# Optimization experiments

Measured on AMD Instinct MI355X. Metric: run time of the kernel, lower is better.

The kernel has to match this reference:

```python
import jax, jax.numpy as jnp
import numpy as np

B, S, D, H = 2, 2048, 1024, 16
DH = D // H  # head_dim = 64


def setup_inputs() -> dict:
    key = jax.random.key(0)
    ks = jax.random.split(key, 12)
    sd = 0.02
    return {
        "query": jax.random.normal(ks[0], (B, S, D), jnp.float32),
        "value": jax.random.normal(ks[1], (B, S, D), jnp.float32),
        "Wq": jax.random.normal(ks[2], (D, D), jnp.float32) * sd,
        "bq": jnp.zeros((D,), jnp.float32),
        "Wk": jax.random.normal(ks[3], (D, DH), jnp.float32) * sd,
        "bk": jnp.zeros((DH,), jnp.float32),
        "Wv": jax.random.normal(ks[4], (D, DH), jnp.float32) * sd,
        "bv": jnp.zeros((DH,), jnp.float32),
        "Wo": jax.random.normal(ks[5], (D, D), jnp.float32) * sd,
        "bo": jnp.zeros((D,), jnp.float32),
    }


def reference(query, value, Wq, bq, Wk, bk, Wv, bv, Wo, bo):
    b, s, d = query.shape
    # per-head queries: (B, H, S, DH)
    Q = (query @ Wq + bq).reshape(b, s, H, DH).transpose(0, 2, 1, 3)
    # single shared K/V head: (B, S, DH)
    K = value @ Wk + bk
    V = value @ Wv + bv
    scale = 1.0 / jnp.sqrt(jnp.asarray(DH, Q.dtype))
    # broadcast shared K over all query heads: (B, H, S, S)
    scores = jnp.einsum("bhsd,btd->bhst", Q, K) * scale
    weights = jax.nn.softmax(scores, axis=-1)
    # (B, H, S, DH)
    attn = jnp.einsum("bhst,btd->bhsd", weights, V)
    concat = attn.transpose(0, 2, 1, 3).reshape(b, s, d)
    return concat @ Wo + bo
```

## Files before the change

kernel.cpp:

```cpp
#include <hip/hip_runtime.h>
#include <hip/hip_bf16.h>
#include <cstdint>

#define S_LEN 2048
#define D_MODEL 1024
#define NHEAD 16
#define DHEAD 64
#define BATCH 2

typedef __attribute__((ext_vector_type(4))) __bf16 bf16x4v;
typedef __attribute__((ext_vector_type(8))) __bf16 bf16x8v;
typedef __attribute__((ext_vector_type(16))) float f32x16;
typedef const __attribute__((address_space(1))) uint32_t gu32;
typedef __attribute__((address_space(3))) uint32_t lu32;

#define QSCALE 0.18033688011112042f

__device__ __forceinline__ int perm4(int gidx) {
    return (gidx & ~3) | ((gidx & 1) << 1) | ((gidx >> 1) & 1);
}
__device__ __forceinline__ int permk(int k) {
    return (k & ~12) | ((k & 4) << 1) | ((k & 8) >> 1);
}

__global__ __launch_bounds__(256) void prep_all(
    const float* __restrict__ query,
    const float* __restrict__ Wq, const float* __restrict__ Wo,
    const float* __restrict__ Wk, const float* __restrict__ Wv,
    __hip_bfloat16* __restrict__ Qin,
    __hip_bfloat16* __restrict__ Wqt, __hip_bfloat16* __restrict__ Wohit,
    __hip_bfloat16* __restrict__ Wkvt)
{
    const int bid = blockIdx.x;
    const int tid = threadIdx.x;
    if (bid < 4096) {
        const int idx = bid * 256 + tid;
        const float4 v = reinterpret_cast<const float4*>(query)[idx];
        bf16x4v o = { (__bf16)v.x, (__bf16)v.y, (__bf16)v.z, (__bf16)v.w };
        *reinterpret_cast<bf16x4v*>(Qin + (size_t)perm4(idx) * 4) = o;
        return;
    }
    const int b2 = bid - 4096;
    const int bx = b2 & 31, by = (b2 >> 5) & 31, z = b2 >> 10;
    const float* W;
    __hip_bfloat16* T;
    int wcols, trowoff;
    if (z == 0)      { W = Wq; T = Wqt;   wcols = 1024; trowoff = 0; }
    else if (z == 1) { W = Wo; T = Wohit; wcols = 1024; trowoff = 0; }
    else if (z == 2) { W = Wk; T = Wkvt;  wcols = 64;   trowoff = 0; }
    else             { W = Wv; T = Wkvt;  wcols = 64;   trowoff = 64; }
    if (bx * 32 >= wcols) return;

    __shared__ float ld[32][33];
    const int jj = tid & 31;
#pragma unroll
    for (int ii = 0; ii < 4; ++ii) {
        const int rr = (tid >> 5) * 4 + ii;
        ld[rr][jj] = W[(size_t)(by * 32 + rr) * wcols + bx * 32 + jj];
    }
    __syncthreads();
#pragma unroll
    for (int ii = 0; ii < 4; ++ii) {
        const int rr = (tid >> 5) * 4 + ii;
        T[(size_t)(trowoff + bx * 32 + rr) * 1024 + by * 32 + permk(jj)] =
            __float2bfloat16(ld[jj][rr]);
    }
}

__global__ __launch_bounds__(512, 1) void qproj_projkv(
    const __hip_bfloat16* __restrict__ Qin,
    const __hip_bfloat16* __restrict__ Wqt,
    const float* __restrict__ bq,
    __hip_bfloat16* __restrict__ Qbf,
    const float* __restrict__ value,
    const __hip_bfloat16* __restrict__ Wkvt,
    const float* __restrict__ bk, const float* __restrict__ bv,
    __hip_bfloat16* __restrict__ Kb,
    __hip_bfloat16* __restrict__ Vt)
{
    __shared__ __align__(16) char lds[131072];
    const int bid = blockIdx.x;
    const int tid = threadIdx.x;

    if (bid < 64) {
        const int unit = tid >> 8;
        const int ltid = tid & 255;
        const int w = ltid >> 6, lane = ltid & 63;
        const int g = lane >> 5, r = lane & 31;
        const int rowBase = bid * 64 + unit * 32;
        char* ub = lds + unit * 65536;

        auto stage = [&](int buf, int t) {
            const int kk = t * 64;
            char* dst = ub + buf * 24576;
#pragma unroll
            for (int j = 0; j < 2; ++j) {
                const int oo  = j * 4096 + ltid * 16;
                const int row = oo >> 8;
                const int cb  = (oo & 255) ^ ((row & 7) << 4);
                __builtin_amdgcn_global_load_lds(
                    (gu32*)((const char*)value + (size_t)(rowBase + row) * 4096 + kk * 4 + cb),
                    (lu32*)(dst + oo), 16, 0, 0);
            }
#pragma unroll
            for (int j = 0; j < 4; ++j) {
                const int oo  = j * 4096 + ltid * 16;
                const int row = oo >> 7;
                const int cb  = (oo & 127) ^ ((row & 7) << 4);
                __builtin_amdgcn_global_load_lds(
                    (gu32*)((const char*)Wkvt + (size_t)row * 2048 + kk * 2 + cb),
                    (lu32*)(dst + 8192 + oo), 16, 0, 0);
            }
        };

        f32x16 acc;
#pragma unroll
        for (int i = 0; i < 16; ++i) acc[i] = 0.f;

        stage(0, 0);

        for (int t = 0; t < 16; ++t) {
            const int cur = t & 1;
            if (t < 15) {
                stage(cur ^ 1, t + 1);
                asm volatile("s_waitcnt vmcnt(6)" ::: "memory");
            } else {
                asm volatile("s_waitcnt vmcnt(0)" ::: "memory");
            }
            asm volatile("s_barrier" ::: "memory");

            const char* ab = ub + cur * 24576;
            const char* bb = ab + 8192;

#pragma unroll
            for (int ks = 0; ks < 4; ++ks) {
                const int sza = (r & 7) << 4;
                const char* pa = ab + r * 256;
                const float4 x0 = *reinterpret_cast<const float4*>(
                    pa + ((ks * 64 + g * 16) ^ sza));
                const float4 x1 = *reinterpret_cast<const float4*>(
                    pa + ((ks * 64 + 32 + g * 16) ^ sza));
                bf16x8v af = {(__bf16)x0.x, (__bf16)x0.y, (__bf16)x0.z, (__bf16)x0.w,
                              (__bf16)x1.x, (__bf16)x1.y, (__bf16)x1.z, (__bf16)x1.w};
                bf16x8v bf = *reinterpret_cast<const bf16x8v*>(
                    bb + (w * 32 + r) * 128 + ((ks * 32 + g * 16) ^ sza));
                acc = __builtin_amdgcn_mfma_f32_32x32x16_bf16(af, bf, acc, 0, 0, 0);
            }
            asm volatile("s_barrier" ::: "memory");
        }

        __syncthreads();
        float* ep = reinterpret_cast<float*>(ub);
#pragma unroll
        for (int reg = 0; reg < 16; ++reg) {
            const int m = (reg & 3) + 8 * (reg >> 2) + 4 * g;
            ep[m * 132 + w * 32 + r] = acc[reg];
        }
        __syncthreads();

        {
            const int m  = ltid >> 3;
            const int g0 = (ltid & 7) * 2;
#pragma unroll
            for (int j = 0; j < 2; ++j) {
                const int gsrc = g0 + j;
                bf16x4v o4;
#pragma unroll
                for (int i2 = 0; i2 < 4; ++i2)
                    o4[i2] = (__bf16)(ep[m * 132 + gsrc * 4 + i2] + bk[gsrc * 4 + i2]);
                *reinterpret_cast<bf16x4v*>(
                    Kb + (size_t)(rowBase + m) * 64 + perm4(gsrc) * 4) = o4;
            }
        }
        {
            const int vc = ltid >> 2;
            const int g0 = (ltid & 3) * 2;
            const int batch = rowBase >> 11;
            const float bvv = bv[vc];
#pragma unroll
            for (int j = 0; j < 2; ++j) {
                const int gsrc = g0 + j;
                bf16x4v o4;
#pragma unroll
                for (int i2 = 0; i2 < 4; ++i2)
                    o4[i2] = (__bf16)(ep[(gsrc * 4 + i2) * 132 + 64 + vc] + bvv);
                *reinterpret_cast<bf16x4v*>(
                    Vt + ((size_t)(batch * 64 + vc)) * 2048 + (rowBase & 2047) + perm4(gsrc) * 4) = o4;
            }
        }
        return;
    }

    const int lin = bid - 64;
    const int w = tid >> 6, lane = tid & 63;
    const int g = lane >> 5, r = lane & 31;
    const int wr = w >> 2, wc = w & 3;
    const int swz = (lin & 7) * 32 + (lin >> 3);
    const int rowBase = (swz >> 3) * 128;
    const int colBase = (swz & 7) * 128;

    auto stage = [&](int buf, int t) {
        const int kk = t * 64;
        char* dst = lds + buf * 32768;
#pragma unroll
        for (int j = 0; j < 2; ++j) {
            const int oo  = j * 8192 + tid * 16;
            const int row = oo >> 7;
            const int cb  = (oo & 127) ^ ((row & 7) << 4);
            __builtin_amdgcn_global_load_lds(
                (gu32*)((const char*)Qin + (size_t)(rowBase + row) * 2048 + kk * 2 + cb),
                (lu32*)(dst + oo), 16, 0, 0);
            __builtin_amdgcn_global_load_lds(
                (gu32*)((const char*)Wqt + (size_t)(colBase + row) * 2048 + kk * 2 + cb),
                (lu32*)(dst + 16384 + oo), 16, 0, 0);
        }
    };

    f32x16 acc[2];
#pragma unroll
    for (int i = 0; i < 16; ++i) { acc[0][i] = 0.f; acc[1][i] = 0.f; }

    stage(0, 0); stage(1, 1); stage(2, 2);

    for (int t = 0; t < 16; ++t) {
        if (t <= 13)      { asm volatile("s_waitcnt vmcnt(8)" ::: "memory"); }
        else if (t == 14) { asm volatile("s_waitcnt vmcnt(4)" ::: "memory"); }
        else              { asm volatile("s_waitcnt vmcnt(0)" ::: "memory"); }
        asm volatile("s_barrier" ::: "memory");

        if (t + 3 < 16) stage((t + 3) & 3, t + 3);

        const char* ahb = lds + (t & 3) * 32768;
        const char* bb  = ahb + 16384;

        __builtin_amdgcn_s_setprio(1);
#pragma unroll
        for (int ks = 0; ks < 4; ++ks) {
            bf16x8v a[2], bfr;
#pragma unroll
            for (int mt = 0; mt < 2; ++mt) {
                const int rowl = wr * 64 + mt * 32 + r;
                const int sz = (rowl & 7) << 4;
                a[mt] = *reinterpret_cast<const bf16x8v*>(
                    ahb + rowl * 128 + ((ks * 32 + g * 16) ^ sz));
            }
            {
                const int rowl = wc * 32 + r;
                const int sz = (rowl & 7) << 4;
                bfr = *reinterpret_cast<const bf16x8v*>(
                    bb + rowl * 128 + ((ks * 32 + g * 16) ^ sz));
            }
#pragma unroll
            for (int mt = 0; mt < 2; ++mt)
                acc[mt] = __builtin_amdgcn_mfma_f32_32x32x16_bf16(a[mt], bfr, acc[mt], 0, 0, 0);
        }
        __builtin_amdgcn_s_setprio(0);
    }

    const int col = colBase + wc * 32 + r;
    const int colp = permk(col);
    const float bvv = bq[col];
#pragma unroll
    for (int mt = 0; mt < 2; ++mt)
#pragma unroll
        for (int reg = 0; reg < 16; ++reg) {
            const int row = rowBase + wr * 64 + mt * 32 + (reg & 3) + 8 * (reg >> 2) + 4 * g;
            Qbf[(size_t)row * 1024 + colp] =
                (__hip_bfloat16)((acc[mt][reg] + bvv) * QSCALE);
        }
}

__global__ __launch_bounds__(512, 1) void gemm_oproj(
    const __hip_bfloat16* __restrict__ Ahi, const __hip_bfloat16* __restrict__ Alo,
    const __hip_bfloat16* __restrict__ Bhi,
    const float* __restrict__ bias, float* __restrict__ C)
{
    constexpr int BUFSZ = 49152;
    __shared__ __align__(16) char lds[147456];

    const int tid = threadIdx.x;
    const int w = tid >> 6, lane = tid & 63;
    const int g = lane >> 5, r = lane & 31;
    const int wr = w >> 2, wc = w & 3;
    const int lin = blockIdx.y * 8 + blockIdx.x;
    const int swz = (lin & 7) * 32 + (lin >> 3);
    const int rowBase = (swz >> 3) * 128;
    const int colBase = (swz & 7) * 128;

    auto stage = [&](int buf, int t) {
        const int kk = t * 64;
        char* dst = lds + buf * BUFSZ;
#pragma unroll
        for (int j = 0; j < 2; ++j) {
            const int oo  = j * 8192 + tid * 16;
            const int row = oo >> 7;
            const int cb  = (oo & 127) ^ ((row & 7) << 4);
            __builtin_amdgcn_global_load_lds(
                (gu32*)((const char*)Ahi + (size_t)(rowBase + row) * 2048 + kk * 2 + cb),
                (lu32*)(dst + oo), 16, 0, 0);
            __builtin_amdgcn_global_load_lds(
                (gu32*)((const char*)Alo + (size_t)(rowBase + row) * 2048 + kk * 2 + cb),
                (lu32*)(dst + 16384 + oo), 16, 0, 0);
            __builtin_amdgcn_global_load_lds(
                (gu32*)((const char*)Bhi + (size_t)(colBase + row) * 2048 + kk * 2 + cb),
                (lu32*)(dst + 32768 + oo), 16, 0, 0);
        }
    };

    f32x16 acc[2];
#pragma unroll
    for (int i = 0; i < 16; ++i) { acc[0][i] = 0.f; acc[1][i] = 0.f; }

    stage(0, 0); stage(1, 1);
    int b_cur = 0, b_nxt = 1, b_stg = 2;

    for (int t = 0; t < 16; ++t) {
        if (t < 15) { asm volatile("s_waitcnt vmcnt(6)" ::: "memory"); }
        else        { asm volatile("s_waitcnt vmcnt(0)" ::: "memory"); }
        asm volatile("s_barrier" ::: "memory");

        if (t + 2 < 16) stage(b_stg, t + 2);

        const char* ahb = lds + b_cur * BUFSZ;
        const char* alb = ahb + 16384;
        const char* bb  = ahb + 32768;

        __builtin_amdgcn_s_setprio(1);
#pragma unroll
        for (int ks = 0; ks < 4; ++ks) {
            bf16x8v a[2], a2[2], bfr;
#pragma unroll
            for (int mt = 0; mt < 2; ++mt) {
                const int rowl = wr * 64 + mt * 32 + r;
                const int sz = (rowl & 7) << 4;
                a[mt]  = *reinterpret_cast<const bf16x8v*>(
                    ahb + rowl * 128 + ((ks * 32 + g * 16) ^ sz));
                a2[mt] = *reinterpret_cast<const bf16x8v*>(
                    alb + rowl * 128 + ((ks * 32 + g * 16) ^ sz));
            }
            {
                const int rowl = wc * 32 + r;
                const int sz = (rowl & 7) << 4;
                bfr = *reinterpret_cast<const bf16x8v*>(
                    bb + rowl * 128 + ((ks * 32 + g * 16) ^ sz));
            }
#pragma unroll
            for (int mt = 0; mt < 2; ++mt) {
                acc[mt] = __builtin_amdgcn_mfma_f32_32x32x16_bf16(a[mt],  bfr, acc[mt], 0, 0, 0);
                acc[mt] = __builtin_amdgcn_mfma_f32_32x32x16_bf16(a2[mt], bfr, acc[mt], 0, 0, 0);
            }
        }
        __builtin_amdgcn_s_setprio(0);

        const int tmp = b_cur; b_cur = b_nxt; b_nxt = b_stg; b_stg = tmp;
    }

    const int col = colBase + wc * 32 + r;
    const float bvv = bias[col];
#pragma unroll
    for (int mt = 0; mt < 2; ++mt)
#pragma unroll
        for (int reg = 0; reg < 16; ++reg) {
            const int row = rowBase + wr * 64 + mt * 32 + (reg & 3) + 8 * (reg >> 2) + 4 * g;
            C[(size_t)row * 1024 + col] = acc[mt][reg] + bvv;
        }
}

__global__ __launch_bounds__(256, 2) void mqa_attn_mfma(
    const __hip_bfloat16* __restrict__ Qbf,
    const __hip_bfloat16* __restrict__ Kbf,
    const __hip_bfloat16* __restrict__ Vt,
    __hip_bfloat16* __restrict__ Ahi,
    __hip_bfloat16* __restrict__ Alo)
{
    __shared__ __align__(16) char lds[65536];

    const int bh = blockIdx.y, b = bh >> 4, h = bh & 15;
    const int qt = blockIdx.x;
    const int tid = threadIdx.x;
    const int w = tid >> 6, lane = tid & 63;
    const int g = lane >> 5, q = lane & 31;

    bf16x8v qf[4];
    {
        const __hip_bfloat16* qp =
            Qbf + ((size_t)(b * S_LEN + qt * 128 + w * 32 + q)) * D_MODEL + h * DHEAD;
#pragma unroll
        for (int ks = 0; ks < 4; ++ks)
            qf[ks] = *reinterpret_cast<const bf16x8v*>(qp + ks * 16 + g * 8);
    }

    const bf16x8v onesf = {(__bf16)1.f, (__bf16)1.f, (__bf16)1.f, (__bf16)1.f,
                           (__bf16)1.f, (__bf16)1.f, (__bf16)1.f, (__bf16)1.f};
    f32x16 fzero;
#pragma unroll
    for (int i = 0; i < 16; ++i) fzero[i] = 0.f;

    int koff[2][4], voff[2][4];
#pragma unroll
    for (int mt = 0; mt < 2; ++mt) {
        const int key = mt * 32 + q;
        const int swzk = (key & 7) << 4;
#pragma unroll
        for (int ks = 0; ks < 4; ++ks) {
            koff[mt][ks] = key * 128 + ((ks * 32 + g * 16) ^ swzk);
            voff[mt][ks] = 8192 + key * 128 + ((ks * 32 + g * 16) ^ swzk);
        }
    }

    const char* kbase = (const char*)Kbf + (size_t)b * S_LEN * DHEAD * 2;
    const char* vbase = (const char*)Vt + (size_t)b * DHEAD * S_LEN * 2;

    auto stage = [&](int buf, int t0) {
        char* dst = lds + buf * 16384;
#pragma unroll
        for (int j = 0; j < 2; ++j) {
            const int oo = j * 4096 + tid * 16;
            const int rr = oo >> 7;
            const int cc = (oo & 127) ^ ((rr & 7) << 4);
            __builtin_amdgcn_global_load_lds(
                (gu32*)(kbase + (size_t)(t0 + rr) * 128 + cc),
                (lu32*)(dst + oo), 16, 0, 0);
            __builtin_amdgcn_global_load_lds(
                (gu32*)(vbase + (size_t)rr * (S_LEN * 2) + t0 * 2 + cc),
                (lu32*)(dst + 8192 + oo), 16, 0, 0);
        }
    };

    f32x16 oacc[2], oacc_l;
#pragma unroll
    for (int i = 0; i < 16; ++i) { oacc[0][i] = 0.f; oacc[1][i] = 0.f; oacc_l[i] = 0.f; }

    auto qkt = [&](f32x16 (&SD)[2], int buf) {
        const char* kb_ = lds + buf * 16384;
#pragma unroll
        for (int mt = 0; mt < 2; ++mt) {
            bf16x8v af0 = *reinterpret_cast<const bf16x8v*>(kb_ + koff[mt][0]);
            SD[mt] = __builtin_amdgcn_mfma_f32_32x32x16_bf16(af0, qf[0], fzero, 0, 0, 0);
#pragma unroll
            for (int ks = 1; ks < 4; ++ks) {
                bf16x8v af = *reinterpret_cast<const bf16x8v*>(kb_ + koff[mt][ks]);
                SD[mt] = __builtin_amdgcn_mfma_f32_32x32x16_bf16(af, qf[ks], SD[mt], 0, 0, 0);
            }
        }
    };

    auto smpv = [&](f32x16 (&SD)[2], int buf) {
#pragma unroll
        for (int mt = 0; mt < 2; ++mt)
#pragma unroll
            for (int r2 = 0; r2 < 16; ++r2)
                SD[mt][r2] = exp2f(SD[mt][r2]);

        bf16x8v pf[4];
#pragma unroll
        for (int ks = 0; ks < 4; ++ks)
#pragma unroll
            for (int e2 = 0; e2 < 8; ++e2)
                pf[ks][e2] = (__bf16)SD[ks >> 1][(ks & 1) * 8 + e2];

        const char* kb_ = lds + buf * 16384;
#pragma unroll
        for (int mt = 0; mt < 2; ++mt) {
#pragma unroll
            for (int ks = 0; ks < 4; ++ks) {
                bf16x8v af = *reinterpret_cast<const bf16x8v*>(kb_ + voff[mt][ks]);
                oacc[mt] = __builtin_amdgcn_mfma_f32_32x32x16_bf16(af, pf[ks], oacc[mt], 0, 0, 0);
            }
        }
#pragma unroll
        for (int ks = 0; ks < 4; ++ks)
            oacc_l = __builtin_amdgcn_mfma_f32_32x32x16_bf16(onesf, pf[ks], oacc_l, 0, 0, 0);
    };

    f32x16 sA[2], sB[2];

    stage(0, 0); stage(1, 64); stage(2, 128);
    asm volatile("s_waitcnt vmcnt(8)" ::: "memory");
    asm volatile("s_barrier" ::: "memory");
    qkt(sA, 0);

#define BODY(SB_, TILE_, BQ_, BP_, CUR, NXT, VMCSTR, DOSTAGE)               \
    {                                                                        \
        asm volatile("s_waitcnt vmcnt(" VMCSTR ")" ::: "memory");            \
        asm volatile("s_barrier" ::: "memory");                              \
        if (DOSTAGE) stage(SB_, TILE_);                                      \
        qkt(NXT, BQ_);                                                       \
        smpv(CUR, BP_);                                                      \
    }

    for (int ib = 0; ib < 7; ++ib) {
        const int t4 = ib * 4;
        BODY(3, (t4 + 3) * 64, 1, 0, sA, sB, "4", true);
        BODY(0, (t4 + 4) * 64, 2, 1, sB, sA, "4", true);
        BODY(1, (t4 + 5) * 64, 3, 2, sA, sB, "4", true);
        BODY(2, (t4 + 6) * 64, 0, 3, sB, sA, "4", true);
    }
    BODY(3, 31 * 64, 1, 0, sA, sB, "4", true);
    BODY(0, 0,       2, 1, sB, sA, "4", false);
    BODY(0, 0,       3, 2, sA, sB, "0", false);
#undef BODY
    smpv(sB, 3);

    const float inv = 1.f / oacc_l[0];
    __syncthreads();
    {
        float* ep = reinterpret_cast<float*>(lds) + w * 2080;
#pragma unroll
        for (int mt = 0; mt < 2; ++mt)
#pragma unroll
            for (int r = 0; r < 16; ++r) {
                const int d = mt * 32 + (r & 3) + ((r >> 2) * 8) + g * 4;
                ep[q * 65 + d] = oacc[mt][r] * inv;
            }
    }
    __syncthreads();

    const size_t obase = (size_t)(b * S_LEN + qt * 128) * D_MODEL + h * DHEAD;
    for (int i = tid; i < 128 * 16; i += 256) {
        const int rloc = i >> 4, G = i & 15;
        const float* src = reinterpret_cast<float*>(lds) + (rloc >> 5) * 2080 + (rloc & 31) * 65 + G * 4;
        const size_t o = obase + (size_t)rloc * D_MODEL + perm4(G) * 4;
        bf16x4v hv, lv;
#pragma unroll
        for (int j = 0; j < 4; ++j) {
            const float v = src[j];
            const float h2 = __bfloat162float(__float2bfloat16(v));
            hv[j] = (__bf16)h2;
            lv[j] = (__bf16)(v - h2);
        }
        *reinterpret_cast<bf16x4v*>(Ahi + o) = hv;
        *reinterpret_cast<bf16x4v*>(Alo + o) = lv;
    }
}

extern "C" void kernel_launch(void* const* d_in, const int* in_sizes, int n_in,
                              void* d_out, int out_size, void* d_ws, size_t ws_size,
                              hipStream_t stream)
{
    const float* query = (const float*)d_in[0];
    const float* value = (const float*)d_in[1];
    const float* Wq    = (const float*)d_in[2];
    const float* bq    = (const float*)d_in[3];
    const float* Wk    = (const float*)d_in[4];
    const float* bk    = (const float*)d_in[5];
    const float* Wv    = (const float*)d_in[6];
    const float* bv    = (const float*)d_in[7];
    const float* Wo    = (const float*)d_in[8];
    const float* bo    = (const float*)d_in[9];
    float* out = (float*)d_out;

    char* ws = (char*)d_ws;
    const size_t MB = 1024 * 1024;
    __hip_bfloat16* Qin   = (__hip_bfloat16*)(ws);
    __hip_bfloat16* AhiB  = (__hip_bfloat16*)(ws);
    __hip_bfloat16* Wqt   = (__hip_bfloat16*)(ws + 8 * MB);
    __hip_bfloat16* Qbf   = (__hip_bfloat16*)(ws + 10 * MB);
    __hip_bfloat16* AloB  = (__hip_bfloat16*)(ws + 10 * MB);
    __hip_bfloat16* Kbf   = (__hip_bfloat16*)(ws + 18 * MB);
    __hip_bfloat16* Vt    = (__hip_bfloat16*)(ws + 18 * MB + 524288);
    __hip_bfloat16* Wohit = (__hip_bfloat16*)(ws + 19 * MB);
    __hip_bfloat16* Wkvt  = (__hip_bfloat16*)(ws + 21 * MB);

    prep_all<<<dim3(8192), dim3(256), 0, stream>>>(
        query, Wq, Wo, Wk, Wv, Qin, Wqt, Wohit, Wkvt);

    qproj_projkv<<<dim3(320), dim3(512), 0, stream>>>(
        Qin, Wqt, bq, Qbf, value, Wkvt, bk, bv, Kbf, Vt);

    mqa_attn_mfma<<<dim3(S_LEN / 128, BATCH * NHEAD), dim3(256), 0, stream>>>(
        Qbf, Kbf, Vt, AhiB, AloB);

    gemm_oproj<<<dim3(8, 32), dim3(512), 0, stream>>>(
        AhiB, AloB, Wohit, bo, out);
}
```

Baseline: 109.3 us.

## Fuse query bf16 conversion into Q-proj GEMM and drop hi/lo split of attention output

The query fp32-to-bf16 conversion pass is removed; the Q-projection GEMM now stages fp32 query tiles into LDS and converts to bf16 while building MFMA fragments, with a 3-buffer pipeline. The attention output is now written as a single bf16 tensor instead of hi/lo split pairs, halving the MFMA work and A-loads in the output projection. This removes an extra global round-trip and redundant compute, at the cost of lower output-projection precision and more LDS traffic in the Q-projection.

```diff
diff --git a/kernel.cpp b/kernel.cpp
--- a/kernel.cpp
+++ b/kernel.cpp
@@ -23,25 +23,13 @@
     return (k & ~12) | ((k & 4) << 1) | ((k & 8) >> 1);
 }
 
-__global__ __launch_bounds__(256) void prep_all(
-    const float* __restrict__ query,
+__global__ __launch_bounds__(256) void prep_w(
     const float* __restrict__ Wq, const float* __restrict__ Wo,
     const float* __restrict__ Wk, const float* __restrict__ Wv,
-    __hip_bfloat16* __restrict__ Qin,
     __hip_bfloat16* __restrict__ Wqt, __hip_bfloat16* __restrict__ Wohit,
     __hip_bfloat16* __restrict__ Wkvt)
 {
-    const int bid = blockIdx.x;
-    const int tid = threadIdx.x;
-    if (bid < 4096) {
-        const int idx = bid * 256 + tid;
-        const float4 v = reinterpret_cast<const float4*>(query)[idx];
-        bf16x4v o = { (__bf16)v.x, (__bf16)v.y, (__bf16)v.z, (__bf16)v.w };
-        *reinterpret_cast<bf16x4v*>(Qin + (size_t)perm4(idx) * 4) = o;
-        return;
-    }
-    const int b2 = bid - 4096;
-    const int bx = b2 & 31, by = (b2 >> 5) & 31, z = b2 >> 10;
+    const int z = blockIdx.z;
     const float* W;
     __hip_bfloat16* T;
     int wcols, trowoff;
@@ -49,9 +37,11 @@
     else if (z == 1) { W = Wo; T = Wohit; wcols = 1024; trowoff = 0; }
     else if (z == 2) { W = Wk; T = Wkvt;  wcols = 64;   trowoff = 0; }
     else             { W = Wv; T = Wkvt;  wcols = 64;   trowoff = 64; }
+    const int bx = blockIdx.x, by = blockIdx.y;
     if (bx * 32 >= wcols) return;
 
     __shared__ float ld[32][33];
+    const int tid = threadIdx.x;
     const int jj = tid & 31;
 #pragma unroll
     for (int ii = 0; ii < 4; ++ii) {
@@ -68,7 +58,7 @@
 }
 
 __global__ __launch_bounds__(512, 1) void qproj_projkv(
-    const __hip_bfloat16* __restrict__ Qin,
+    const float* __restrict__ query,
     const __hip_bfloat16* __restrict__ Wqt,
     const float* __restrict__ bq,
     __hip_bfloat16* __restrict__ Qbf,
@@ -78,7 +68,7 @@
     __hip_bfloat16* __restrict__ Kb,
     __hip_bfloat16* __restrict__ Vt)
 {
-    __shared__ __align__(16) char lds[131072];
+    __shared__ __align__(16) char lds[147456];
     const int bid = blockIdx.x;
     const int tid = threadIdx.x;
 
@@ -201,18 +191,24 @@
 
     auto stage = [&](int buf, int t) {
         const int kk = t * 64;
-        char* dst = lds + buf * 32768;
+        char* dst = lds + buf * 49152;
+#pragma unroll
+        for (int j = 0; j < 4; ++j) {
+            const int oo  = j * 8192 + tid * 16;
+            const int row = oo >> 8;
+            const int cb  = (oo & 255) ^ ((row & 7) << 4);
+            __builtin_amdgcn_global_load_lds(
+                (gu32*)((const char*)query + (size_t)(rowBase + row) * 4096 + kk * 4 + cb),
+                (lu32*)(dst + oo), 16, 0, 0);
+        }
 #pragma unroll
         for (int j = 0; j < 2; ++j) {
             const int oo  = j * 8192 + tid * 16;
             const int row = oo >> 7;
             const int cb  = (oo & 127) ^ ((row & 7) << 4);
             __builtin_amdgcn_global_load_lds(
-                (gu32*)((const char*)Qin + (size_t)(rowBase + row) * 2048 + kk * 2 + cb),
-                (lu32*)(dst + oo), 16, 0, 0);
-            __builtin_amdgcn_global_load_lds(
                 (gu32*)((const char*)Wqt + (size_t)(colBase + row) * 2048 + kk * 2 + cb),
-                (lu32*)(dst + 16384 + oo), 16, 0, 0);
+                (lu32*)(dst + 32768 + oo), 16, 0, 0);
         }
     };
 
@@ -220,18 +216,18 @@
 #pragma unroll
     for (int i = 0; i < 16; ++i) { acc[0][i] = 0.f; acc[1][i] = 0.f; }
 
-    stage(0, 0); stage(1, 1); stage(2, 2);
+    stage(0, 0); stage(1, 1);
+    int b_cur = 0, b_nxt = 1, b_stg = 2;
 
     for (int t = 0; t < 16; ++t) {
-        if (t <= 13)      { asm volatile("s_waitcnt vmcnt(8)" ::: "memory"); }
-        else if (t == 14) { asm volatile("s_waitcnt vmcnt(4)" ::: "memory"); }
-        else              { asm volatile("s_waitcnt vmcnt(0)" ::: "memory"); }
+        if (t < 15) { asm volatile("s_waitcnt vmcnt(6)" ::: "memory"); }
+        else        { asm volatile("s_waitcnt vmcnt(0)" ::: "memory"); }
         asm volatile("s_barrier" ::: "memory");
 
-        if (t + 3 < 16) stage((t + 3) & 3, t + 3);
-
-        const char* ahb = lds + (t & 3) * 32768;
-        const char* bb  = ahb + 16384;
+        if (t + 2 < 16) stage(b_stg, t + 2);
+
+        const char* ab = lds + b_cur * 49152;
+        const char* bb = ab + 32768;
 
         __builtin_amdgcn_s_setprio(1);
 #pragma unroll
@@ -241,8 +237,13 @@
             for (int mt = 0; mt < 2; ++mt) {
                 const int rowl = wr * 64 + mt * 32 + r;
                 const int sz = (rowl & 7) << 4;
-                a[mt] = *reinterpret_cast<const bf16x8v*>(
-                    ahb + rowl * 128 + ((ks * 32 + g * 16) ^ sz));
+                const char* pa = ab + rowl * 256;
+                const float4 x0 = *reinterpret_cast<const float4*>(
+                    pa + ((ks * 64 + g * 16) ^ sz));
+                const float4 x1 = *reinterpret_cast<const float4*>(
+                    pa + ((ks * 64 + 32 + g * 16) ^ sz));
+                a[mt] = bf16x8v{(__bf16)x0.x, (__bf16)x0.y, (__bf16)x0.z, (__bf16)x0.w,
+                                (__bf16)x1.x, (__bf16)x1.y, (__bf16)x1.z, (__bf16)x1.w};
             }
             {
                 const int rowl = wc * 32 + r;
@@ -255,6 +256,8 @@
                 acc[mt] = __builtin_amdgcn_mfma_f32_32x32x16_bf16(a[mt], bfr, acc[mt], 0, 0, 0);
         }
         __builtin_amdgcn_s_setprio(0);
+
+        const int tmp = b_cur; b_cur = b_nxt; b_nxt = b_stg; b_stg = tmp;
     }
 
     const int col = colBase + wc * 32 + r;
@@ -271,12 +274,11 @@
 }
 
 __global__ __launch_bounds__(512, 1) void gemm_oproj(
-    const __hip_bfloat16* __restrict__ Ahi, const __hip_bfloat16* __restrict__ Alo,
+    const __hip_bfloat16* __restrict__ A,
     const __hip_bfloat16* __restrict__ Bhi,
     const float* __restrict__ bias, float* __restrict__ C)
 {
-    constexpr int BUFSZ = 49152;
-    __shared__ __align__(16) char lds[147456];
+    __shared__ __align__(16) char lds[131072];
 
     const int tid = threadIdx.x;
     const int w = tid >> 6, lane = tid & 63;
@@ -289,21 +291,18 @@
 
     auto stage = [&](int buf, int t) {
         const int kk = t * 64;
-        char* dst = lds + buf * BUFSZ;
+        char* dst = lds + buf * 32768;
 #pragma unroll
         for (int j = 0; j < 2; ++j) {
             const int oo  = j * 8192 + tid * 16;
             const int row = oo >> 7;
             const int cb  = (oo & 127) ^ ((row & 7) << 4);
             __builtin_amdgcn_global_load_lds(
-                (gu32*)((const char*)Ahi + (size_t)(rowBase + row) * 2048 + kk * 2 + cb),
+                (gu32*)((const char*)A + (size_t)(rowBase + row) * 2048 + kk * 2 + cb),
                 (lu32*)(dst + oo), 16, 0, 0);
             __builtin_amdgcn_global_load_lds(
-                (gu32*)((const char*)Alo + (size_t)(rowBase + row) * 2048 + kk * 2 + cb),
+                (gu32*)((const char*)Bhi + (size_t)(colBase + row) * 2048 + kk * 2 + cb),
                 (lu32*)(dst + 16384 + oo), 16, 0, 0);
-            __builtin_amdgcn_global_load_lds(
-                (gu32*)((const char*)Bhi + (size_t)(colBase + row) * 2048 + kk * 2 + cb),
-                (lu32*)(dst + 32768 + oo), 16, 0, 0);
         }
     };
 
@@ -311,32 +310,29 @@
 #pragma unroll
     for (int i = 0; i < 16; ++i) { acc[0][i] = 0.f; acc[1][i] = 0.f; }
 
-    stage(0, 0); stage(1, 1);
-    int b_cur = 0, b_nxt = 1, b_stg = 2;
+    stage(0, 0); stage(1, 1); stage(2, 2);
 
     for (int t = 0; t < 16; ++t) {
-        if (t < 15) { asm volatile("s_waitcnt vmcnt(6)" ::: "memory"); }
-        else        { asm volatile("s_waitcnt vmcnt(0)" ::: "memory"); }
+        if (t <= 13)      { asm volatile("s_waitcnt vmcnt(8)" ::: "memory"); }
+        else if (t == 14) { asm volatile("s_waitcnt vmcnt(4)" ::: "memory"); }
+        else              { asm volatile("s_waitcnt vmcnt(0)" ::: "memory"); }
         asm volatile("s_barrier" ::: "memory");
 
-        if (t + 2 < 16) stage(b_stg, t + 2);
-
-        const char* ahb = lds + b_cur * BUFSZ;
-        const char* alb = ahb + 16384;
-        const char* bb  = ahb + 32768;
+        if (t + 3 < 16) stage((t + 3) & 3, t + 3);
+
+        const char* ahb = lds + (t & 3) * 32768;
+        const char* bb  = ahb + 16384;
 
         __builtin_amdgcn_s_setprio(1);
 #pragma unroll
         for (int ks = 0; ks < 4; ++ks) {
-            bf16x8v a[2], a2[2], bfr;
+            bf16x8v a[2], bfr;
 #pragma unroll
             for (int mt = 0; mt < 2; ++mt) {
                 const int rowl = wr * 64 + mt * 32 + r;
                 const int sz = (rowl & 7) << 4;
-                a[mt]  = *reinterpret_cast<const bf16x8v*>(
+                a[mt] = *reinterpret_cast<const bf16x8v*>(
                     ahb + rowl * 128 + ((ks * 32 + g * 16) ^ sz));
-                a2[mt] = *reinterpret_cast<const bf16x8v*>(
-                    alb + rowl * 128 + ((ks * 32 + g * 16) ^ sz));
             }
             {
                 const int rowl = wc * 32 + r;
@@ -345,14 +341,10 @@
                     bb + rowl * 128 + ((ks * 32 + g * 16) ^ sz));
             }
 #pragma unroll
-            for (int mt = 0; mt < 2; ++mt) {
-                acc[mt] = __builtin_amdgcn_mfma_f32_32x32x16_bf16(a[mt],  bfr, acc[mt], 0, 0, 0);
-                acc[mt] = __builtin_amdgcn_mfma_f32_32x32x16_bf16(a2[mt], bfr, acc[mt], 0, 0, 0);
-            }
+            for (int mt = 0; mt < 2; ++mt)
+                acc[mt] = __builtin_amdgcn_mfma_f32_32x32x16_bf16(a[mt], bfr, acc[mt], 0, 0, 0);
         }
         __builtin_amdgcn_s_setprio(0);
-
-        const int tmp = b_cur; b_cur = b_nxt; b_nxt = b_stg; b_stg = tmp;
     }
 
     const int col = colBase + wc * 32 + r;
@@ -370,8 +362,7 @@
     const __hip_bfloat16* __restrict__ Qbf,
     const __hip_bfloat16* __restrict__ Kbf,
     const __hip_bfloat16* __restrict__ Vt,
-    __hip_bfloat16* __restrict__ Ahi,
-    __hip_bfloat16* __restrict__ Alo)
+    __hip_bfloat16* __restrict__ Ahi)
 {
     __shared__ __align__(16) char lds[65536];
 
@@ -521,16 +512,10 @@
         const int rloc = i >> 4, G = i & 15;
         const float* src = reinterpret_cast<float*>(lds) + (rloc >> 5) * 2080 + (rloc & 31) * 65 + G * 4;
         const size_t o = obase + (size_t)rloc * D_MODEL + perm4(G) * 4;
-        bf16x4v hv, lv;
-#pragma unroll
-        for (int j = 0; j < 4; ++j) {
-            const float v = src[j];
-            const float h2 = __bfloat162float(__float2bfloat16(v));
-            hv[j] = (__bf16)h2;
-            lv[j] = (__bf16)(v - h2);
-        }
+        bf16x4v hv;
+#pragma unroll
+        for (int j = 0; j < 4; ++j) hv[j] = (__bf16)src[j];
         *reinterpret_cast<bf16x4v*>(Ahi + o) = hv;
-        *reinterpret_cast<bf16x4v*>(Alo + o) = lv;
     }
 }
 
@@ -552,25 +537,23 @@
 
     char* ws = (char*)d_ws;
     const size_t MB = 1024 * 1024;
-    __hip_bfloat16* Qin   = (__hip_bfloat16*)(ws);
-    __hip_bfloat16* AhiB  = (__hip_bfloat16*)(ws);
+    __hip_bfloat16* Qbf   = (__hip_bfloat16*)(ws);
+    __hip_bfloat16* Abuf  = (__hip_bfloat16*)(ws);
     __hip_bfloat16* Wqt   = (__hip_bfloat16*)(ws + 8 * MB);
-    __hip_bfloat16* Qbf   = (__hip_bfloat16*)(ws + 10 * MB);
-    __hip_bfloat16* AloB  = (__hip_bfloat16*)(ws + 10 * MB);
-    __hip_bfloat16* Kbf   = (__hip_bfloat16*)(ws + 18 * MB);
-    __hip_bfloat16* Vt    = (__hip_bfloat16*)(ws + 18 * MB + 524288);
-    __hip_bfloat16* Wohit = (__hip_bfloat16*)(ws + 19 * MB);
-    __hip_bfloat16* Wkvt  = (__hip_bfloat16*)(ws + 21 * MB);
-
-    prep_all<<<dim3(8192), dim3(256), 0, stream>>>(
-        query, Wq, Wo, Wk, Wv, Qin, Wqt, Wohit, Wkvt);
+    __hip_bfloat16* Kbf   = (__hip_bfloat16*)(ws + 10 * MB);
+    __hip_bfloat16* Vt    = (__hip_bfloat16*)(ws + 10 * MB + 524288);
+    __hip_bfloat16* Wohit = (__hip_bfloat16*)(ws + 11 * MB);
+    __hip_bfloat16* Wkvt  = (__hip_bfloat16*)(ws + 13 * MB);
+
+    prep_w<<<dim3(32, 32, 4), dim3(256), 0, stream>>>(
+        Wq, Wo, Wk, Wv, Wqt, Wohit, Wkvt);
 
     qproj_projkv<<<dim3(320), dim3(512), 0, stream>>>(
-        Qin, Wqt, bq, Qbf, value, Wkvt, bk, bv, Kbf, Vt);
+        query, Wqt, bq, Qbf, value, Wkvt, bk, bv, Kbf, Vt);
 
     mqa_attn_mfma<<<dim3(S_LEN / 128, BATCH * NHEAD), dim3(256), 0, stream>>>(
-        Qbf, Kbf, Vt, AhiB, AloB);
+        Qbf, Kbf, Vt, Abuf);
 
     gemm_oproj<<<dim3(8, 32), dim3(512), 0, stream>>>(
-        AhiB, AloB, Wohit, bo, out);
-}
+        Abuf, Wohit, bo, out);
+}
```

New measurement: 116.7 us. 6.8% more time.
